# Performance work log

Hardware: AMD Instinct MI355X
Metric: run time of the kernel (lower is better)

Reference implementation:

```python
import jax, jax.numpy as jnp
import numpy as np

N = 20000          # nodes
E = 320000         # edges (avg degree 16)
G = 256            # graphs in batch
NUM_TACTICS = 1000
NUM_TYPES = 3
TYPE_D = 32
TAC_D = 64
H = 512
IN_D = TYPE_D + TAC_D  # 96


def setup_inputs() -> dict:
    key = jax.random.key(0)
    ks = jax.random.split(key, 16)
    node_type = jax.random.randint(ks[0], (N,), 0, NUM_TYPES)
    # tactic id in {-1, 0..num_tactics-1}
    node_tactic_id = jax.random.randint(ks[1], (N,), 0, NUM_TACTICS + 1) - 1
    edge_index = jax.random.randint(ks[2], (2, E), 0, N)
    batch = jnp.sort(jax.random.randint(ks[3], (N,), 0, G))
    s = 0.02
    p = {
        'type_emb': jax.random.normal(ks[4], (NUM_TYPES, TYPE_D), jnp.float32) * s,
        'tactic_emb': jax.random.normal(ks[5], (NUM_TACTICS + 1, TAC_D), jnp.float32) * s,
        'W1l': jax.random.normal(ks[6], (H, IN_D), jnp.float32) * s,
        'b1l': jnp.zeros((H,), jnp.float32),
        'W1r': jax.random.normal(ks[7], (H, IN_D), jnp.float32) * s,
        'W2l': jax.random.normal(ks[8], (H, H), jnp.float32) * s,
        'b2l': jnp.zeros((H,), jnp.float32),
        'W2r': jax.random.normal(ks[9], (H, H), jnp.float32) * s,
        'Wc1': jax.random.normal(ks[10], (H, H), jnp.float32) * s,
        'bc1': jnp.zeros((H,), jnp.float32),
        'Wc2': jax.random.normal(ks[11], (NUM_TACTICS, H), jnp.float32) * s,
        'bc2': jnp.zeros((NUM_TACTICS,), jnp.float32),
    }
    return dict(node_type=node_type, node_tactic_id=node_tactic_id,
                edge_index=edge_index, batch=batch, **p)


def _sage_conv(x, src, dst, Wl, bl, Wr):
    # PyG SAGEConv (aggr='mean'): out = lin_l(mean_{j in N(i)} x_j) + lin_r(x_i)
    msg = x[src]                                              # [E, D]
    ssum = jax.ops.segment_sum(msg, dst, num_segments=N)      # [N, D]
    cnt = jax.ops.segment_sum(jnp.ones((src.shape[0],), x.dtype), dst,
                              num_segments=N)                 # [N]
    agg = ssum / jnp.maximum(cnt, 1.0)[:, None]
    return agg @ Wl.T + bl + x @ Wr.T


def reference(node_type, node_tactic_id, edge_index, batch,
              type_emb, tactic_emb, W1l, b1l, W1r, W2l, b2l, W2r,
              Wc1, bc1, Wc2, bc2):
    t_type = type_emb[node_type]                              # [N, 32]
    shifted = jnp.clip(node_tactic_id + 1, 0, NUM_TACTICS)
    t_tac = tactic_emb[shifted]                               # [N, 64]
    x = jnp.concatenate([t_type, t_tac], axis=-1)             # [N, 96]

    src, dst = edge_index[0], edge_index[1]
    x = jax.nn.relu(_sage_conv(x, src, dst, W1l, b1l, W1r))   # [N, H]
    x = _sage_conv(x, src, dst, W2l, b2l, W2r)                # [N, H]

    # global mean pool over graphs
    gsum = jax.ops.segment_sum(x, batch, num_segments=G)      # [G, H]
    gcnt = jax.ops.segment_sum(jnp.ones((N,), x.dtype), batch, num_segments=G)
    graph_repr = gsum / jnp.maximum(gcnt, 1.0)[:, None]

    h = jax.nn.relu(graph_repr @ Wc1.T + bc1)
    logits = h @ Wc2.T + bc2                                  # [G, num_tactics]
    return logits
```

## Files before the change

### kernel.cpp

```cpp
#include <hip/hip_runtime.h>

#define N_NODES 20000
#define N_EDGES 320000
#define NGRAPH  256
#define NTAC    1000
#define HD      512
#define NC      25
#define KCH     800

typedef __attribute__((ext_vector_type(8))) short bf16x8;
typedef __attribute__((ext_vector_type(4))) short short4v;
typedef __attribute__((ext_vector_type(4))) float f32x4;

__device__ __forceinline__ short f2bf(float f) {
  union { float f; unsigned u; } v; v.f = f;
  unsigned r = v.u + 0x7FFFu + ((v.u >> 16) & 1u);
  return (short)(r >> 16);
}
__device__ __forceinline__ float bf2f(short s) {
  union { unsigned u; float f; } v;
  v.u = ((unsigned)(unsigned short)s) << 16;
  return v.f;
}
__device__ __forceinline__ bf16x8 cast8(const float* p) {
  float4 v0 = *reinterpret_cast<const float4*>(p);
  float4 v1 = *reinterpret_cast<const float4*>(p + 4);
  bf16x8 o;
  o[0] = f2bf(v0.x); o[1] = f2bf(v0.y); o[2] = f2bf(v0.z); o[3] = f2bf(v0.w);
  o[4] = f2bf(v1.x); o[5] = f2bf(v1.y); o[6] = f2bf(v1.z); o[7] = f2bf(v1.w);
  return o;
}
__device__ __forceinline__ void gload16(const void* g, void* l) {
  __builtin_amdgcn_global_load_lds((const __attribute__((address_space(1))) void*)g,
                                   (__attribute__((address_space(3))) void*)l,
                                   16, 0, 0);
}

__global__ void k_front(const float* __restrict__ Wc1, const float* __restrict__ Wc2,
                        short* __restrict__ WC1B, short* __restrict__ WC2B,
                        const float* __restrict__ W1l, const float* __restrict__ W1r,
                        short* __restrict__ BC1,
                        const float* __restrict__ W2l, const float* __restrict__ W2r,
                        short* __restrict__ BC2,
                        const int* __restrict__ ntype, const int* __restrict__ ntac,
                        const float* __restrict__ temb, const float* __restrict__ tacemb,
                        short* __restrict__ A1,
                        const int* __restrict__ dst, int* __restrict__ deg,
                        const int* __restrict__ batch, int* __restrict__ rstart,
                        float* __restrict__ COEF, short* __restrict__ COEFB) {
  int idx = blockIdx.x * 256 + threadIdx.x;
  const int S0 = HD * HD / 8;
  const int S1 = NTAC * HD / 8;
  const int S2 = HD * 192 / 8;
  const int S3 = HD * 1024 / 8;
  const int S4 = N_NODES * 24;
  const int S5 = N_EDGES;
  const int S6 = N_NODES;
  const int S7 = NGRAPH * N_NODES / 4;
  const int S8 = NGRAPH * N_NODES / 8;
  if (idx < S0) {
    *reinterpret_cast<bf16x8*>(&WC1B[idx * 8]) = cast8(&Wc1[idx * 8]);
  } else if ((idx -= S0) < S1) {
    *reinterpret_cast<bf16x8*>(&WC2B[idx * 8]) = cast8(&Wc2[idx * 8]);
  } else if ((idx -= S1) < S2) {
    int n = idx / 24, k8 = idx - n * 24;
    const float* s = (k8 < 12) ? &W1l[(size_t)n * 96 + k8 * 8]
                               : &W1r[(size_t)n * 96 + (k8 - 12) * 8];
    *reinterpret_cast<bf16x8*>(&BC1[(size_t)n * 192 + k8 * 8]) = cast8(s);
  } else if ((idx -= S2) < S3) {
    int n = idx >> 7, k8 = idx & 127;
    const float* s = (k8 < 64) ? &W2l[(size_t)n * 512 + k8 * 8]
                               : &W2r[(size_t)n * 512 + (k8 - 64) * 8];
    *reinterpret_cast<bf16x8*>(&BC2[(size_t)n * 1024 + k8 * 8]) = cast8(s);
  } else if ((idx -= S3) < S4) {
    int node = idx / 24;
    int j = idx - node * 24;
    float4 v;
    int col;
    if (j < 8) {
      int t = ntype[node];
      v = *reinterpret_cast<const float4*>(&temb[t * 32 + j * 4]);
      col = j * 4;
    } else {
      int s = ntac[node] + 1;
      s = s < 0 ? 0 : (s > NTAC ? NTAC : s);
      v = *reinterpret_cast<const float4*>(&tacemb[s * 64 + (j - 8) * 4]);
      col = 32 + (j - 8) * 4;
    }
    short4v o = {f2bf(v.x), f2bf(v.y), f2bf(v.z), f2bf(v.w)};
    *reinterpret_cast<short4v*>(&A1[(size_t)node * 192 + 96 + col]) = o;
  } else if ((idx -= S4) < S5) {
    atomicAdd(&deg[dst[idx]], 1);
  } else if ((idx -= S5) < S6) {
    int i = idx;
    int b = batch[i];
    int bp = (i == 0) ? -1 : batch[i - 1];
    for (int g = bp + 1; g <= b; ++g) rstart[g] = i;
    if (i == N_NODES - 1)
      for (int g = b + 1; g <= NGRAPH; ++g) rstart[g] = N_NODES;
  } else if ((idx -= S6) < S7) {
    float4 z = {0.f, 0.f, 0.f, 0.f};
    *reinterpret_cast<float4*>(&COEF[(size_t)idx * 4]) = z;
  } else if ((idx -= S7) < S8) {
    bf16x8 z = {0, 0, 0, 0, 0, 0, 0, 0};
    *reinterpret_cast<bf16x8*>(&COEFB[(size_t)NGRAPH * N_NODES + (size_t)idx * 8]) = z;
  }
}

__global__ __launch_bounds__(1024) void k_scan(const int* __restrict__ deg,
                                               int* __restrict__ rowstart) {
  __shared__ int partial[1024];
  const int t = threadIdx.x;
  const int CH = (N_NODES + 1023) / 1024;
  int s = 0;
  for (int i = 0; i < CH; ++i) {
    int idx = t * CH + i;
    if (idx < N_NODES) s += deg[idx];
  }
  partial[t] = s;
  __syncthreads();
  for (int off = 1; off < 1024; off <<= 1) {
    int v = (t >= off) ? partial[t - off] : 0;
    __syncthreads();
    partial[t] += v;
    __syncthreads();
  }
  int run = (t == 0) ? 0 : partial[t - 1];
  for (int i = 0; i < CH; ++i) {
    int idx = t * CH + i;
    if (idx < N_NODES) { rowstart[idx] = run; run += deg[idx]; }
  }
  if (t == 1023) rowstart[N_NODES] = run;
}

__global__ void k_scatter(const int* __restrict__ src, const int* __restrict__ dst,
                          const int* __restrict__ rows, int* __restrict__ cur,
                          int* __restrict__ esrc, const int* __restrict__ batch,
                          const int* __restrict__ rstart,
                          float* __restrict__ COEF, short* __restrict__ COEFB) {
  int idx = blockIdx.x * 256 + threadIdx.x;
  if (idx < N_EDGES) {
    int d = dst[idx];
    int p = rows[d] + atomicAdd(&cur[d], 1);
    int sj = src[idx];
    esrc[p] = sj;
    int g = batch[d];
    float invd = 1.0f / (float)max(rows[d + 1] - rows[d], 1);
    float invg = 1.0f / (float)max(rstart[g + 1] - rstart[g], 1);
    atomicAdd(&COEF[(size_t)g * N_NODES + sj], invd * invg);
  } else if ((idx -= N_EDGES) < N_NODES) {
    int j = idx;
    int g = batch[j];
    float invg = 1.0f / (float)max(rstart[g + 1] - rstart[g], 1);
    COEFB[(size_t)(NGRAPH + g) * N_NODES + j] = f2bf(invg);
  }
}

__global__ __launch_bounds__(256) void k_mid(
    const float* __restrict__ COEF, short* __restrict__ COEFB,
    const int* __restrict__ rowstart, const int* __restrict__ esrc,
    short* __restrict__ A1) {
  int idx = blockIdx.x * 256 + threadIdx.x;
  const int SC = NGRAPH * N_NODES / 8;
  if (idx < SC) {
    int r = idx / 2500, k8 = (idx - r * 2500) * 8;
    *reinterpret_cast<bf16x8*>(&COEFB[(size_t)r * N_NODES + k8]) =
        cast8(&COEF[(size_t)r * N_NODES + k8]);
    return;
  }
  idx -= SC;
  if (idx >= N_NODES * 24) return;
  int node = idx / 24;
  int c = (idx - node * 24) * 4;
  const int s0 = rowstart[node], s1 = rowstart[node + 1];
  float a0 = 0.f, a1 = 0.f, a2 = 0.f, a3 = 0.f;
  for (int i = s0; i < s1; ++i) {
    int nbr = esrc[i];
    short4v v = *reinterpret_cast<const short4v*>(&A1[(size_t)nbr * 192 + 96 + c]);
    a0 += bf2f(v[0]); a1 += bf2f(v[1]); a2 += bf2f(v[2]); a3 += bf2f(v[3]);
  }
  const float inv = 1.0f / fmaxf((float)(s1 - s0), 1.0f);
  short4v o = {f2bf(a0 * inv), f2bf(a1 * inv), f2bf(a2 * inv), f2bf(a3 * inv)};
  *reinterpret_cast<short4v*>(&A1[(size_t)node * 192 + c]) = o;
}

__global__ __launch_bounds__(256) void k_gemm_l1(
    const short* __restrict__ A, const short* __restrict__ B,
    const float* __restrict__ bias, short* __restrict__ X1T, int nxp) {
  constexpr int K = 192;
  __shared__ short smem[32768];
  const int lin = blockIdx.x;
  const int pnl = (lin & 7) + ((lin >> 5) << 3);
  const int cbk = (lin >> 3) & 3;
  if (pnl >= nxp) return;
  const int m0 = pnl * 128, n0 = cbk * 128;
  const int t = threadIdx.x;
  const int l = t & 63, wid = t >> 6;
  const int wr = (wid >> 1) * 64, wc = (wid & 1) * 64;
  const int fr = l & 15, fs = l >> 4;

  f32x4 acc[4][4];
#pragma unroll
  for (int a = 0; a < 4; ++a)
#pragma unroll
    for (int b = 0; b < 4; ++b) acc[a][b] = (f32x4){0.f, 0.f, 0.f, 0.f};

  const int idx0 = t, r0 = idx0 >> 2, sp0 = idx0 & 3;
  const int sl0 = (sp0 - (r0 >> 1)) & 3;
  const int idx1 = t + 256, r1 = idx1 >> 2, sp1 = idx1 & 3;
  const int sl1 = (sp1 - (r1 >> 1)) & 3;
  int rowA0 = m0 + r0; rowA0 = rowA0 < N_NODES ? rowA0 : N_NODES - 1;
  int rowA1 = m0 + r1; rowA1 = rowA1 < N_NODES ? rowA1 : N_NODES - 1;
  const short* Ap0 = A + (size_t)rowA0 * K + sl0 * 8;
  const short* Ap1 = A + (size_t)rowA1 * K + sl1 * 8;
  const short* Bp0 = B + (size_t)(n0 + r0) * K + sl0 * 8;
  const short* Bp1 = B + (size_t)(n0 + r1) * K + sl1 * 8;
  constexpr int NK = K / 32;

#define STAGE1(bo, k0)                                 \
  gload16(Ap0 + (k0), &smem[(bo) + idx0 * 8]);         \
  gload16(Bp0 + (k0), &smem[(bo) + 4096 + idx0 * 8]);  \
  gload16(Ap1 + (k0), &smem[(bo) + idx1 * 8]);         \
  gload16(Bp1 + (k0), &smem[(bo) + 4096 + idx1 * 8]);

#define COMPUTE1(bo) {                                                             \
  bf16x8 av[4], bv[4];                                                             \
  _Pragma("unroll")                                                                \
  for (int mi = 0; mi < 4; ++mi) {                                                 \
    const int r = wr + mi * 16 + fr;                                               \
    av[mi] = *reinterpret_cast<const bf16x8*>(                                     \
        &smem[(bo) + r * 32 + ((fs + (r >> 1)) & 3) * 8]);                         \
  }                                                                                \
  _Pragma("unroll")                                                                \
  for (int ni = 0; ni < 4; ++ni) {                                                 \
    const int r = wc + ni * 16 + fr;                                               \
    bv[ni] = *reinterpret_cast<const bf16x8*>(                                     \
        &smem[(bo) + 4096 + r * 32 + ((fs + (r >> 1)) & 3) * 8]);                  \
  }                                                                                \
  _Pragma("unroll")                                                                \
  for (int mi = 0; mi < 4; ++mi)                                                   \
    _Pragma("unroll")                                                              \
    for (int ni = 0; ni < 4; ++ni)                                                 \
      acc[mi][ni] = __builtin_amdgcn_mfma_f32_16x16x32_bf16(av[mi], bv[ni],        \
                                                            acc[mi][ni], 0, 0, 0); }

  STAGE1(0, 0)
  STAGE1(8192, 32)
  STAGE1(16384, 64)
#pragma unroll
  for (int k = 0; k < NK; ++k) {
    if (k + 2 <= NK - 1)      { asm volatile("s_waitcnt vmcnt(8)" ::: "memory"); }
    else if (k + 1 <= NK - 1) { asm volatile("s_waitcnt vmcnt(4)" ::: "memory"); }
    else                      { asm volatile("s_waitcnt vmcnt(0)" ::: "memory"); }
    __builtin_amdgcn_s_barrier();
    if (k + 3 < NK) { STAGE1(((k + 3) & 3) * 8192, (k + 3) * 32) }
    COMPUTE1((k & 3) * 8192)
  }
#undef STAGE1
#undef COMPUTE1

  __syncthreads();
#pragma unroll
  for (int ni = 0; ni < 4; ++ni) {
    const int colL = wc + ni * 16 + fr;
    const float bb = bias[n0 + colL];
#pragma unroll
    for (int mi = 0; mi < 4; ++mi) {
      const f32x4 c = acc[mi][ni];
#pragma unroll
      for (int i = 0; i < 4; ++i) {
        const int rowL = wr + mi * 16 + fs * 4 + i;
        smem[colL * 136 + rowL] = f2bf(fmaxf(c[i] + bb, 0.f));
      }
    }
  }
  __syncthreads();
#pragma unroll
  for (int q = 0; q < 8; ++q) {
    const int it = q * 256 + t;
    const int cr = it >> 4, n8 = (it & 15) << 3;
    if (m0 + n8 < N_NODES)
      *reinterpret_cast<bf16x8*>(&X1T[(size_t)(n0 + cr) * N_NODES + m0 + n8]) =
          *reinterpret_cast<const bf16x8*>(&smem[cr * 136 + n8]);
  }
}

__global__ __launch_bounds__(256) void k_bigemm(
    const short* __restrict__ A,
    const short* __restrict__ B,
    float* __restrict__ CP) {
  __shared__ short smem[32768];
  const int bx = blockIdx.x;
  const int grp = (bx & 7) + ((bx >> 5) << 3);
  const int sib = (bx >> 3) & 3;
  if (grp >= NC * 4) return;
  const int chunk = grp >> 2, panel = grp & 3;
  const int m0 = panel * 128, n0 = sib * 128;
  const int kb = chunk * KCH;
  const int t = threadIdx.x;
  const int l = t & 63, wid = t >> 6;
  const int wr = (wid >> 1) * 64, wc = (wid & 1) * 64;
  const int fr = l & 15, fs = l >> 4;

  f32x4 acc[4][4];
#pragma unroll
  for (int a = 0; a < 4; ++a)
#pragma unroll
    for (int b = 0; b < 4; ++b) acc[a][b] = (f32x4){0.f, 0.f, 0.f, 0.f};

  const int idx0 = t, r0 = idx0 >> 2, sp0 = idx0 & 3;
  const int sl0 = (sp0 - (r0 >> 1)) & 3;
  const int idx1 = t + 256, r1 = idx1 >> 2, sp1 = idx1 & 3;
  const int sl1 = (sp1 - (r1 >> 1)) & 3;
  const short* Ap0 = A + (size_t)(m0 + r0) * N_NODES + kb + sl0 * 8;
  const short* Ap1 = A + (size_t)(m0 + r1) * N_NODES + kb + sl1 * 8;
  const short* Bp0 = B + (size_t)(n0 + r0) * N_NODES + kb + sl0 * 8;
  const short* Bp1 = B + (size_t)(n0 + r1) * N_NODES + kb + sl1 * 8;
  constexpr int NK = KCH / 32;

#define STAGE2(bo, k0)                                 \
  gload16(Ap0 + (k0), &smem[(bo) + idx0 * 8]);         \
  gload16(Bp0 + (k0), &smem[(bo) + 4096 + idx0 * 8]);  \
  gload16(Ap1 + (k0), &smem[(bo) + idx1 * 8]);         \
  gload16(Bp1 + (k0), &smem[(bo) + 4096 + idx1 * 8]);

#define COMPUTE2(bo) {                                                             \
  bf16x8 av[4], bv[4];                                                             \
  _Pragma("unroll")                                                                \
  for (int mi = 0; mi < 4; ++mi) {                                                 \
    const int r = wr + mi * 16 + fr;                                               \
    av[mi] = *reinterpret_cast<const bf16x8*>(                                     \
        &smem[(bo) + r * 32 + ((fs + (r >> 1)) & 3) * 8]);                         \
  }                                                                                \
  _Pragma("unroll")                                                                \
  for (int ni = 0; ni < 4; ++ni) {                                                 \
    const int r = wc + ni * 16 + fr;                                               \
    bv[ni] = *reinterpret_cast<const bf16x8*>(                                     \
        &smem[(bo) + 4096 + r * 32 + ((fs + (r >> 1)) & 3) * 8]);                  \
  }                                                                                \
  _Pragma("unroll")                                                                \
  for (int mi = 0; mi < 4; ++mi)                                                   \
    _Pragma("unroll")                                                              \
    for (int ni = 0; ni < 4; ++ni)                                                 \
      acc[mi][ni] = __builtin_amdgcn_mfma_f32_16x16x32_bf16(av[mi], bv[ni],        \
                                                            acc[mi][ni], 0, 0, 0); }

  STAGE2(0, 0)
  STAGE2(8192, 32)
  STAGE2(16384, 64)
  for (int k = 0; k < NK; ++k) {
    if (k + 2 <= NK - 1)      { asm volatile("s_waitcnt vmcnt(8)" ::: "memory"); }
    else if (k + 1 <= NK - 1) { asm volatile("s_waitcnt vmcnt(4)" ::: "memory"); }
    else                      { asm volatile("s_waitcnt vmcnt(0)" ::: "memory"); }
    __builtin_amdgcn_s_barrier();
    if (k + 3 < NK) { STAGE2(((k + 3) & 3) * 8192, (k + 3) * 32) }
    COMPUTE2((k & 3) * 8192)
  }
#undef STAGE2
#undef COMPUTE2

  __syncthreads();
  float* smemf = reinterpret_cast<float*>(smem);
  for (int half = 0; half < 2; ++half) {
    if (wr == half * 64) {
#pragma unroll
      for (int ni = 0; ni < 4; ++ni) {
        const int colL = wc + ni * 16 + fr;
#pragma unroll
        for (int mi = 0; mi < 4; ++mi) {
          const f32x4 c = acc[mi][ni];
#pragma unroll
          for (int i = 0; i < 4; ++i) {
            const int row = mi * 16 + fs * 4 + i;
            smemf[row * 132 + colL] = c[i];
          }
        }
      }
    }
    __syncthreads();
#pragma unroll
    for (int q = 0; q < 8; ++q) {
      const int it = q * 256 + t;
      const int row = it >> 5, c4 = (it & 31) * 4;
      *reinterpret_cast<f32x4*>(
          &CP[((size_t)chunk * 512 + m0 + half * 64 + row) * 512 + n0 + c4]) =
          *reinterpret_cast<const f32x4*>(&smemf[row * 132 + c4]);
    }
    __syncthreads();
  }
}

__global__ __launch_bounds__(256) void k_redP(const float* __restrict__ CP,
                                              short* __restrict__ PB) {
  int it = blockIdx.x * 256 + threadIdx.x;
  int r = it >> 7, c4 = (it & 127) * 4;
  f32x4 s = (f32x4){0.f, 0.f, 0.f, 0.f};
  for (int ch = 0; ch < NC; ++ch) {
    f32x4 v = *reinterpret_cast<const f32x4*>(&CP[((size_t)ch * 512 + r) * 512 + c4]);
    s[0] += v[0]; s[1] += v[1]; s[2] += v[2]; s[3] += v[3];
  }
  int g = r & 255, off = (r >> 8) * 512;
  short4v o = {f2bf(s[0]), f2bf(s[1]), f2bf(s[2]), f2bf(s[3])};
  *reinterpret_cast<short4v*>(&PB[(size_t)g * 1024 + off + c4]) = o;
}

template<int K, bool RELU, bool F32OUT>
__device__ __forceinline__ void cls_gemm(
    const short* __restrict__ A, const short* __restrict__ B,
    const float* __restrict__ bias,
    short* __restrict__ outS, int ostride, float* __restrict__ outF) {
  __shared__ short smem[32768];
  const int bx = blockIdx.x;
  const int m0 = (bx & 1) * 128;
  const int n0 = (bx >> 1) * 128;
  const int t = threadIdx.x;
  const int l = t & 63, wid = t >> 6;
  const int wr = (wid >> 1) * 64, wc = (wid & 1) * 64;
  const int fr = l & 15, fs = l >> 4;

  f32x4 acc[4][4];
#pragma unroll
  for (int a = 0; a < 4; ++a)
#pragma unroll
    for (int b = 0; b < 4; ++b) acc[a][b] = (f32x4){0.f, 0.f, 0.f, 0.f};

  const int idx0 = t, r0 = idx0 >> 2, sp0 = idx0 & 3;
  const int sl0 = (sp0 - (r0 >> 1)) & 3;
  const int idx1 = t + 256, r1 = idx1 >> 2, sp1 = idx1 & 3;
  const int sl1 = (sp1 - (r1 >> 1)) & 3;
  const short* Ap0 = A + (size_t)(m0 + r0) * K + sl0 * 8;
  const short* Ap1 = A + (size_t)(m0 + r1) * K + sl1 * 8;
  const short* Bp0 = B + (size_t)(n0 + r0) * K + sl0 * 8;
  const short* Bp1 = B + (size_t)(n0 + r1) * K + sl1 * 8;
  constexpr int NK = K / 32;

#define STAGE3(bo, k0)                                 \
  gload16(Ap0 + (k0), &smem[(bo) + idx0 * 8]);         \
  gload16(Bp0 + (k0), &smem[(bo) + 4096 + idx0 * 8]);  \
  gload16(Ap1 + (k0), &smem[(bo) + idx1 * 8]);         \
  gload16(Bp1 + (k0), &smem[(bo) + 4096 + idx1 * 8]);

#define COMPUTE3(bo) {                                                             \
  bf16x8 av[4], bv[4];                                                             \
  _Pragma("unroll")                                                                \
  for (int mi = 0; mi < 4; ++mi) {                                                 \
    const int r = wr + mi * 16 + fr;                                               \
    av[mi] = *reinterpret_cast<const bf16x8*>(                                     \
        &smem[(bo) + r * 32 + ((fs + (r >> 1)) & 3) * 8]);                         \
  }                                                                                \
  _Pragma("unroll")                                                                \
  for (int ni = 0; ni < 4; ++ni) {                                                 \
    const int r = wc + ni * 16 + fr;                                               \
    bv[ni] = *reinterpret_cast<const bf16x8*>(                                     \
        &smem[(bo) + 4096 + r * 32 + ((fs + (r >> 1)) & 3) * 8]);                  \
  }                                                                                \
  _Pragma("unroll")                                                                \
  for (int mi = 0; mi < 4; ++mi)                                                   \
    _Pragma("unroll")                                                              \
    for (int ni = 0; ni < 4; ++ni)                                                 \
      acc[mi][ni] = __builtin_amdgcn_mfma_f32_16x16x32_bf16(av[mi], bv[ni],        \
                                                            acc[mi][ni], 0, 0, 0); }

  STAGE3(0, 0)
  STAGE3(8192, 32)
  STAGE3(16384, 64)
  for (int k = 0; k < NK; ++k) {
    if (k + 2 <= NK - 1)      { asm volatile("s_waitcnt vmcnt(8)" ::: "memory"); }
    else if (k + 1 <= NK - 1) { asm volatile("s_waitcnt vmcnt(4)" ::: "memory"); }
    else                      { asm volatile("s_waitcnt vmcnt(0)" ::: "memory"); }
    __builtin_amdgcn_s_barrier();
    if (k + 3 < NK) { STAGE3(((k + 3) & 3) * 8192, (k + 3) * 32) }
    COMPUTE3((k & 3) * 8192)
  }
#undef STAGE3
#undef COMPUTE3

  __syncthreads();
  if constexpr (!F32OUT) {
#pragma unroll
    for (int ni = 0; ni < 4; ++ni) {
      const int colL = wc + ni * 16 + fr;
      const float bb = bias[n0 + colL];
#pragma unroll
      for (int mi = 0; mi < 4; ++mi) {
        const f32x4 c = acc[mi][ni];
#pragma unroll
        for (int i = 0; i < 4; ++i) {
          const int rowL = wr + mi * 16 + fs * 4 + i;
          float v = c[i] + bb;
          if (RELU) v = fmaxf(v, 0.f);
          smem[rowL * 136 + colL] = f2bf(v);
        }
      }
    }
    __syncthreads();
#pragma unroll
    for (int pz = 0; pz < 8; ++pz) {
      const int idx = pz * 256 + t;
      const int row = idx >> 4, c8 = (idx & 15) << 3;
      *reinterpret_cast<bf16x8*>(&outS[(size_t)(m0 + row) * ostride + n0 + c8]) =
          *reinterpret_cast<const bf16x8*>(&smem[row * 136 + c8]);
    }
  } else {
    float* smemf = reinterpret_cast<float*>(smem);
    for (int half = 0; half < 2; ++half) {
      if (wr == half * 64) {
#pragma unroll
        for (int ni = 0; ni < 4; ++ni) {
          const int colL = wc + ni * 16 + fr;
          const float bb = bias[n0 + colL];
#pragma unroll
          for (int mi = 0; mi < 4; ++mi) {
            const f32x4 c = acc[mi][ni];
#pragma unroll
            for (int i = 0; i < 4; ++i) {
              const int row = mi * 16 + fs * 4 + i;
              smemf[row * 132 + colL] = c[i] + bb;
            }
          }
        }
      }
      __syncthreads();
#pragma unroll
      for (int q = 0; q < 8; ++q) {
        const int it = q * 256 + t;
        const int row = it >> 5, c4 = (it & 31) * 4;
        if (n0 + c4 < NTAC)
          *reinterpret_cast<f32x4*>(
              &outF[(size_t)(m0 + half * 64 + row) * NTAC + n0 + c4]) =
              *reinterpret_cast<const f32x4*>(&smemf[row * 132 + c4]);
      }
      __syncthreads();
    }
  }
}

__global__ __launch_bounds__(256) void k_cls1(
    const short* __restrict__ A, const short* __restrict__ B,
    const float* __restrict__ bias, short* __restrict__ outS) {
  cls_gemm<1024, false, false>(A, B, bias, outS, 512, nullptr);
}
__global__ __launch_bounds__(256) void k_cls2(
    const short* __restrict__ A, const short* __restrict__ B,
    const float* __restrict__ bias, short* __restrict__ outS) {
  cls_gemm<512, true, false>(A, B, bias, outS, 512, nullptr);
}
__global__ __launch_bounds__(256) void k_cls3(
    const short* __restrict__ A, const short* __restrict__ B,
    const float* __restrict__ bias, float* __restrict__ outF) {
  cls_gemm<512, false, true>(A, B, bias, nullptr, 0, outF);
}

extern "C" void kernel_launch(void* const* d_in, const int* in_sizes, int n_in,
                              void* d_out, int out_size, void* d_ws, size_t ws_size,
                              hipStream_t stream) {
  const int*   node_type = (const int*)d_in[0];
  const int*   node_tac  = (const int*)d_in[1];
  const int*   edge      = (const int*)d_in[2];
  const int*   batch     = (const int*)d_in[3];
  const float* temb      = (const float*)d_in[4];
  const float* tacemb    = (const float*)d_in[5];
  const float* W1l       = (const float*)d_in[6];
  const float* b1l       = (const float*)d_in[7];
  const float* W1r       = (const float*)d_in[8];
  const float* W2l       = (const float*)d_in[9];
  const float* b2l       = (const float*)d_in[10];
  const float* W2r       = (const float*)d_in[11];
  const float* Wc1       = (const float*)d_in[12];
  const float* bc1       = (const float*)d_in[13];
  const float* Wc2       = (const float*)d_in[14];
  const float* bc2       = (const float*)d_in[15];
  const int* src = edge;
  const int* dst = edge + N_EDGES;

  char* p = (char*)d_ws;
  int*   DEG    = (int*)p;    p += N_NODES * 4;
  int*   CUR    = (int*)p;    p += N_NODES * 4;
  size_t zero_bytes = (size_t)(2 * N_NODES) * 4;
  int*   ROWS   = (int*)p;    p += (N_NODES + 4) * 4;
  int*   RSTART = (int*)p;    p += (NGRAPH + 4) * 4;
  int*   ESRC   = (int*)p;    p += N_EDGES * 4;
  short* A1     = (short*)p;  p += (size_t)N_NODES * 192 * 2;
  short* X1T    = (short*)p;  p += (size_t)HD * N_NODES * 2;
  float* COEF   = (float*)p;  p += (size_t)NGRAPH * N_NODES * 4;
  short* COEFB  = (short*)p;  p += (size_t)2 * NGRAPH * N_NODES * 2;
  float* CP     = (float*)p;  p += (size_t)NC * 512 * 512 * 4;
  short* PB     = (short*)p;  p += NGRAPH * 1024 * 2;
  short* GRB    = (short*)p;  p += NGRAPH * HD * 2;
  short* HSB    = (short*)p;  p += NGRAPH * HD * 2;
  short* BC1    = (short*)p;  p += HD * 192 * 2;
  short* BC2    = (short*)p;  p += HD * 1024 * 2;
  short* WC1B   = (short*)p;  p += HD * HD * 2;
  short* WC2B   = (short*)p;  p += (size_t)1024 * HD * 2;

  hipMemsetAsync(d_ws, 0, zero_bytes, stream);

  const int front_items = HD * HD / 8 + NTAC * HD / 8 + HD * 192 / 8 +
                          HD * 1024 / 8 + N_NODES * 24 + N_EDGES + N_NODES +
                          NGRAPH * N_NODES / 4 + NGRAPH * N_NODES / 8;
  k_front<<<(front_items + 255) / 256, 256, 0, stream>>>(
      Wc1, Wc2, WC1B, WC2B, W1l, W1r, BC1, W2l, W2r, BC2,
      node_type, node_tac, temb, tacemb, A1, dst, DEG, batch, RSTART, COEF, COEFB);

  k_scan<<<1, 1024, 0, stream>>>(DEG, ROWS);
  k_scatter<<<(N_EDGES + N_NODES + 255) / 256, 256, 0, stream>>>(
      src, dst, ROWS, CUR, ESRC, batch, RSTART, COEF, COEFB);

  const int mid_items = NGRAPH * N_NODES / 8 + N_NODES * 24;
  k_mid<<<(mid_items + 255) / 256, 256, 0, stream>>>(COEF, COEFB, ROWS, ESRC, A1);

  const int NXP = (N_NODES + 127) / 128;
  k_gemm_l1<<<640, 256, 0, stream>>>(A1, BC1, b1l, X1T, NXP);

  k_bigemm<<<416, 256, 0, stream>>>(COEFB, X1T, CP);
  k_redP<<<256, 256, 0, stream>>>(CP, PB);
  k_cls1<<<8, 256, 0, stream>>>(PB, BC2, b2l, GRB);
  k_cls2<<<8, 256, 0, stream>>>(GRB, WC1B, bc1, HSB);
  k_cls3<<<16, 256, 0, stream>>>(HSB, WC2B, bc2, (float*)d_out);
}
```

Measured before the change: 202.4 us.

## Replace dense graph-mean pooling GEMM rows with segmented reduction over sorted batch

New measurement: 212.1 us. 4.8% more time.

```diff
diff --git a/kernel.cpp b/kernel.cpp
--- a/kernel.cpp
+++ b/kernel.cpp
@@ -45,19 +45,18 @@
                         const int* __restrict__ ntype, const int* __restrict__ ntac,
                         const float* __restrict__ temb, const float* __restrict__ tacemb,
                         short* __restrict__ A1,
-                        const int* __restrict__ dst, int* __restrict__ deg,
+                        int* __restrict__ deg,
                         const int* __restrict__ batch, int* __restrict__ rstart,
-                        float* __restrict__ COEF, short* __restrict__ COEFB) {
+                        float* __restrict__ COEF) {
   int idx = blockIdx.x * 256 + threadIdx.x;
   const int S0 = HD * HD / 8;
   const int S1 = NTAC * HD / 8;
   const int S2 = HD * 192 / 8;
   const int S3 = HD * 1024 / 8;
   const int S4 = N_NODES * 24;
-  const int S5 = N_EDGES;
-  const int S6 = N_NODES;
-  const int S7 = NGRAPH * N_NODES / 4;
-  const int S8 = NGRAPH * N_NODES / 8;
+  const int S5 = N_NODES;
+  const int S6 = NGRAPH * N_NODES / 4;
+  const int S7 = N_NODES / 4;
   if (idx < S0) {
     *reinterpret_cast<bf16x8*>(&WC1B[idx * 8]) = cast8(&Wc1[idx * 8]);
   } else if ((idx -= S0) < S1) {
@@ -90,21 +89,24 @@
     short4v o = {f2bf(v.x), f2bf(v.y), f2bf(v.z), f2bf(v.w)};
     *reinterpret_cast<short4v*>(&A1[(size_t)node * 192 + 96 + col]) = o;
   } else if ((idx -= S4) < S5) {
-    atomicAdd(&deg[dst[idx]], 1);
-  } else if ((idx -= S5) < S6) {
     int i = idx;
     int b = batch[i];
     int bp = (i == 0) ? -1 : batch[i - 1];
     for (int g = bp + 1; g <= b; ++g) rstart[g] = i;
     if (i == N_NODES - 1)
       for (int g = b + 1; g <= NGRAPH; ++g) rstart[g] = N_NODES;
-  } else if ((idx -= S6) < S7) {
+  } else if ((idx -= S5) < S6) {
     float4 z = {0.f, 0.f, 0.f, 0.f};
     *reinterpret_cast<float4*>(&COEF[(size_t)idx * 4]) = z;
-  } else if ((idx -= S7) < S8) {
-    bf16x8 z = {0, 0, 0, 0, 0, 0, 0, 0};
-    *reinterpret_cast<bf16x8*>(&COEFB[(size_t)NGRAPH * N_NODES + (size_t)idx * 8]) = z;
-  }
+  } else if ((idx -= S6) < S7) {
+    int4 z = {0, 0, 0, 0};
+    *reinterpret_cast<int4*>(&deg[idx * 4]) = z;
+  }
+}
+
+__global__ void k_degree(const int* __restrict__ dst, int* __restrict__ deg) {
+  int e = blockIdx.x * 256 + threadIdx.x;
+  if (e < N_EDGES) atomicAdd(&deg[dst[e]], 1);
 }
 
 __global__ __launch_bounds__(1024) void k_scan(const int* __restrict__ deg,
@@ -134,26 +136,21 @@
 }
 
 __global__ void k_scatter(const int* __restrict__ src, const int* __restrict__ dst,
-                          const int* __restrict__ rows, int* __restrict__ cur,
+                          const int* __restrict__ rows, int* __restrict__ deg,
                           int* __restrict__ esrc, const int* __restrict__ batch,
                           const int* __restrict__ rstart,
-                          float* __restrict__ COEF, short* __restrict__ COEFB) {
+                          float* __restrict__ COEF) {
   int idx = blockIdx.x * 256 + threadIdx.x;
-  if (idx < N_EDGES) {
-    int d = dst[idx];
-    int p = rows[d] + atomicAdd(&cur[d], 1);
-    int sj = src[idx];
-    esrc[p] = sj;
-    int g = batch[d];
-    float invd = 1.0f / (float)max(rows[d + 1] - rows[d], 1);
-    float invg = 1.0f / (float)max(rstart[g + 1] - rstart[g], 1);
-    atomicAdd(&COEF[(size_t)g * N_NODES + sj], invd * invg);
-  } else if ((idx -= N_EDGES) < N_NODES) {
-    int j = idx;
-    int g = batch[j];
-    float invg = 1.0f / (float)max(rstart[g + 1] - rstart[g], 1);
-    COEFB[(size_t)(NGRAPH + g) * N_NODES + j] = f2bf(invg);
-  }
+  if (idx >= N_EDGES) return;
+  int d = dst[idx];
+  int old = atomicSub(&deg[d], 1);
+  int p = rows[d + 1] - old;
+  int sj = src[idx];
+  esrc[p] = sj;
+  int g = batch[d];
+  float invd = 1.0f / (float)max(rows[d + 1] - rows[d], 1);
+  float invg = 1.0f / (float)max(rstart[g + 1] - rstart[g], 1);
+  atomicAdd(&COEF[(size_t)g * N_NODES + sj], invd * invg);
 }
 
 __global__ __launch_bounds__(256) void k_mid(
@@ -293,8 +290,8 @@
   const int bx = blockIdx.x;
   const int grp = (bx & 7) + ((bx >> 5) << 3);
   const int sib = (bx >> 3) & 3;
-  if (grp >= NC * 4) return;
-  const int chunk = grp >> 2, panel = grp & 3;
+  if (grp >= NC * 2) return;
+  const int chunk = grp >> 1, panel = grp & 1;
   const int m0 = panel * 128, n0 = sib * 128;
   const int kb = chunk * KCH;
   const int t = threadIdx.x;
@@ -383,7 +380,7 @@
       const int it = q * 256 + t;
       const int row = it >> 5, c4 = (it & 31) * 4;
       *reinterpret_cast<f32x4*>(
-          &CP[((size_t)chunk * 512 + m0 + half * 64 + row) * 512 + n0 + c4]) =
+          &CP[((size_t)chunk * 256 + m0 + half * 64 + row) * 512 + n0 + c4]) =
           *reinterpret_cast<const f32x4*>(&smemf[row * 132 + c4]);
     }
     __syncthreads();
@@ -393,15 +390,32 @@
 __global__ __launch_bounds__(256) void k_redP(const float* __restrict__ CP,
                                               short* __restrict__ PB) {
   int it = blockIdx.x * 256 + threadIdx.x;
-  int r = it >> 7, c4 = (it & 127) * 4;
+  int g = it >> 7, c4 = (it & 127) * 4;
   f32x4 s = (f32x4){0.f, 0.f, 0.f, 0.f};
   for (int ch = 0; ch < NC; ++ch) {
-    f32x4 v = *reinterpret_cast<const f32x4*>(&CP[((size_t)ch * 512 + r) * 512 + c4]);
+    f32x4 v = *reinterpret_cast<const f32x4*>(&CP[((size_t)ch * 256 + g) * 512 + c4]);
     s[0] += v[0]; s[1] += v[1]; s[2] += v[2]; s[3] += v[3];
   }
-  int g = r & 255, off = (r >> 8) * 512;
   short4v o = {f2bf(s[0]), f2bf(s[1]), f2bf(s[2]), f2bf(s[3])};
-  *reinterpret_cast<short4v*>(&PB[(size_t)g * 1024 + off + c4]) = o;
+  *reinterpret_cast<short4v*>(&PB[(size_t)g * 1024 + c4]) = o;
+}
+
+__global__ __launch_bounds__(256) void k_poolX(const short* __restrict__ X1T,
+                                               const int* __restrict__ rstart,
+                                               short* __restrict__ PB) {
+  const int g = blockIdx.x, quarter = blockIdx.y;
+  const int t = threadIdx.x, w = t >> 6, l = t & 63;
+  const int s0 = rstart[g], s1 = rstart[g + 1];
+  const float inv = 1.0f / fmaxf((float)(s1 - s0), 1.0f);
+  for (int i = 0; i < 32; ++i) {
+    const int c = quarter * 128 + w * 32 + i;
+    const short* row = &X1T[(size_t)c * N_NODES];
+    float s = 0.f;
+    for (int j = s0 + l; j < s1; j += 64) s += bf2f(row[j]);
+#pragma unroll
+    for (int off = 32; off > 0; off >>= 1) s += __shfl_down(s, off);
+    if (l == 0) PB[(size_t)g * 1024 + 512 + c] = f2bf(s * inv);
+  }
 }
 
 template<int K, bool RELU, bool F32OUT>
@@ -575,16 +589,14 @@
 
   char* p = (char*)d_ws;
   int*   DEG    = (int*)p;    p += N_NODES * 4;
-  int*   CUR    = (int*)p;    p += N_NODES * 4;
-  size_t zero_bytes = (size_t)(2 * N_NODES) * 4;
   int*   ROWS   = (int*)p;    p += (N_NODES + 4) * 4;
   int*   RSTART = (int*)p;    p += (NGRAPH + 4) * 4;
   int*   ESRC   = (int*)p;    p += N_EDGES * 4;
   short* A1     = (short*)p;  p += (size_t)N_NODES * 192 * 2;
   short* X1T    = (short*)p;  p += (size_t)HD * N_NODES * 2;
   float* COEF   = (float*)p;  p += (size_t)NGRAPH * N_NODES * 4;
-  short* COEFB  = (short*)p;  p += (size_t)2 * NGRAPH * N_NODES * 2;
-  float* CP     = (float*)p;  p += (size_t)NC * 512 * 512 * 4;
+  short* COEFB  = (short*)p;  p += (size_t)NGRAPH * N_NODES * 2;
+  float* CP     = (float*)p;  p += (size_t)NC * 256 * 512 * 4;
   short* PB     = (short*)p;  p += NGRAPH * 1024 * 2;
   short* GRB    = (short*)p;  p += NGRAPH * HD * 2;
   short* HSB    = (short*)p;  p += NGRAPH * HD * 2;
@@ -593,18 +605,17 @@
   short* WC1B   = (short*)p;  p += HD * HD * 2;
   short* WC2B   = (short*)p;  p += (size_t)1024 * HD * 2;
 
-  hipMemsetAsync(d_ws, 0, zero_bytes, stream);
-
   const int front_items = HD * HD / 8 + NTAC * HD / 8 + HD * 192 / 8 +
-                          HD * 1024 / 8 + N_NODES * 24 + N_EDGES + N_NODES +
-                          NGRAPH * N_NODES / 4 + NGRAPH * N_NODES / 8;
+                          HD * 1024 / 8 + N_NODES * 24 + N_NODES +
+                          NGRAPH * N_NODES / 4 + N_NODES / 4;
   k_front<<<(front_items + 255) / 256, 256, 0, stream>>>(
       Wc1, Wc2, WC1B, WC2B, W1l, W1r, BC1, W2l, W2r, BC2,
-      node_type, node_tac, temb, tacemb, A1, dst, DEG, batch, RSTART, COEF, COEFB);
-
+      node_type, node_tac, temb, tacemb, A1, DEG, batch, RSTART, COEF);
+
+  k_degree<<<N_EDGES / 256, 256, 0, stream>>>(dst, DEG);
   k_scan<<<1, 1024, 0, stream>>>(DEG, ROWS);
-  k_scatter<<<(N_EDGES + N_NODES + 255) / 256, 256, 0, stream>>>(
-      src, dst, ROWS, CUR, ESRC, batch, RSTART, COEF, COEFB);
+  k_scatter<<<N_EDGES / 256, 256, 0, stream>>>(src, dst, ROWS, DEG, ESRC,
+                                               batch, RSTART, COEF);
 
   const int mid_items = NGRAPH * N_NODES / 8 + N_NODES * 24;
   k_mid<<<(mid_items + 255) / 256, 256, 0, stream>>>(COEF, COEFB, ROWS, ESRC, A1);
@@ -612,8 +623,9 @@
   const int NXP = (N_NODES + 127) / 128;
   k_gemm_l1<<<640, 256, 0, stream>>>(A1, BC1, b1l, X1T, NXP);
 
-  k_bigemm<<<416, 256, 0, stream>>>(COEFB, X1T, CP);
-  k_redP<<<256, 256, 0, stream>>>(CP, PB);
+  k_bigemm<<<224, 256, 0, stream>>>(COEFB, X1T, CP);
+  k_redP<<<128, 256, 0, stream>>>(CP, PB);
+  k_poolX<<<dim3(NGRAPH, 4), 256, 0, stream>>>(X1T, RSTART, PB);
   k_cls1<<<8, 256, 0, stream>>>(PB, BC2, b2l, GRB);
   k_cls2<<<8, 256, 0, stream>>>(GRB, WC1B, bc1, HSB);
   k_cls3<<<16, 256, 0, stream>>>(HSB, WC2B, bc2, (float*)d_out);
```
